# Performance work log

Measured on AMD Instinct MI355X. Metric: run time of the kernel, lower is better.

## Reference

```python
import jax, jax.numpy as jnp
import numpy as np

D_MODEL = 1024
EXPERT_SIZE = 512
N_EXPERTS = 8
GROUP_SIZE = 32
BATCH = 32
SEQ = 2048
TEMPERATURE = 1.0


def setup_inputs() -> dict:
    key = jax.random.key(0)
    k_x, k_l1, k_l2, k_c = jax.random.split(key, 4)
    x = jax.random.normal(k_x, (BATCH, SEQ, D_MODEL), dtype=jnp.float32)
    # truncated-normal-style init approximated with normal scaled by 1/sqrt(fan_in)
    lin1 = jax.random.normal(k_l1, (N_EXPERTS, D_MODEL, EXPERT_SIZE), dtype=jnp.float32) * (D_MODEL ** -0.5)
    lin2 = jax.random.normal(k_l2, (N_EXPERTS, EXPERT_SIZE, D_MODEL), dtype=jnp.float32) * (EXPERT_SIZE ** -0.5)
    controller = jax.random.normal(k_c, (D_MODEL, N_EXPERTS), dtype=jnp.float32) * (D_MODEL ** -0.5)
    return {"x": x, "lin1": lin1, "lin2": lin2, "controller": controller}


def reference(x, lin1, lin2, controller):
    B, S, D = x.shape
    # group_tokens: sparsity_dim=0 -> transpose to (S, B, D), split batch into groups
    xg = jnp.transpose(x, (1, 0, 2)).reshape(S, B // GROUP_SIZE, GROUP_SIZE, D)  # (s, g, k, d)
    # controller logits, softmax over the group (token) axis k (dim=-2)
    logits = jnp.einsum("sgkd,de->sgke", xg, controller) / TEMPERATURE
    merge_w = jax.nn.softmax(logits, axis=-2)  # (s, g, k, e)
    emit_w = merge_w  # default: emit softmax over tokens, same temp -> reuse
    # merge: weighted sum of tokens per expert
    merged = jnp.einsum("sgke,sgkd->sged", merge_w, xg)  # (s, g, e, d)
    # per-expert MLP
    h = jax.nn.relu(jnp.einsum("sged,edf->sgef", merged, lin1))  # (s, g, e, f)
    expert_out = jnp.einsum("sgef,efd->sged", h, lin2)  # (s, g, e, d)
    # emit back to tokens
    out = jnp.einsum("sgke,sged->sgkd", emit_w, expert_out)  # (s, g, k, d)
    # redistribute: (S, B, D) -> (B, S, D)
    return jnp.transpose(out.reshape(S, B, D), (1, 0, 2))
```

## Files before the change

### kernel.cpp

```cpp
#include <hip/hip_runtime.h>
#include <hip/hip_bf16.h>

#define SS 2048
#define BB 32
#define DD 1024
#define FF 512
#define EE 8

typedef __attribute__((ext_vector_type(8))) short short8;
typedef __attribute__((ext_vector_type(8))) unsigned short ushort8v;
typedef __attribute__((ext_vector_type(4))) unsigned short ushort4v;
typedef __attribute__((ext_vector_type(4))) float f32x4;

__device__ inline unsigned short f2bf(float f) {
  union { float f; unsigned u; } v; v.f = f;
  return (unsigned short)((v.u + 0x7FFFu + ((v.u >> 16) & 1u)) >> 16);
}
__device__ inline float bf2f(unsigned short h) {
  union { unsigned u; float f; } v; v.u = ((unsigned)h) << 16;
  return v.f;
}

__global__ __launch_bounds__(256) void transpose_bf16(
    const float* __restrict__ in, unsigned short* __restrict__ out, int K, int N) {
  __shared__ float tile[32][33];
  int e = blockIdx.z;
  const float* inp = in + (size_t)e * K * N;
  unsigned short* outp = out + (size_t)e * K * N;
  int k0 = blockIdx.x * 32, n0 = blockIdx.y * 32;
  int tx = threadIdx.x;
  int ty = threadIdx.y;
#pragma unroll
  for (int i = 0; i < 4; i++) {
    int k = ty + i * 8;
    tile[k][tx] = inp[(size_t)(k0 + k) * N + n0 + tx];
  }
  __syncthreads();
#pragma unroll
  for (int i = 0; i < 4; i++) {
    int n = ty + i * 8;
    outp[(size_t)(n0 + n) * K + k0 + tx] = f2bf(tile[tx][n]);
  }
}

__global__ __launch_bounds__(512) void ctrl_merge(
    const float* __restrict__ x,
    const float* __restrict__ ctrl,
    unsigned short* __restrict__ merged,
    float* __restrict__ mw) {
  int s = blockIdx.x;
  int t = threadIdx.x;
  int lane = t & 63, w = t >> 6;

  __shared__ float cs[EE][DD];
  __shared__ unsigned short xs[BB][DD];
  __shared__ float wl[BB][EE];

  for (int i = t; i < DD * EE; i += 512) {
    int e2 = i >> 10, d = i & 1023;
    cs[e2][d] = ctrl[(size_t)d * EE + e2];
  }
  __syncthreads();

  float acc[4][8] = {};
#pragma unroll
  for (int i = 0; i < 4; i++) {
    int dbase = lane * 4 + i * 256;
    float4 c4[8];
#pragma unroll
    for (int e2 = 0; e2 < 8; e2++) c4[e2] = *(const float4*)&cs[e2][dbase];
#pragma unroll
    for (int kk = 0; kk < 4; kk++) {
      int k = (w << 2) + kk;
      float4 xv = *(const float4*)&x[((size_t)k * SS + s) * DD + dbase];
      ushort4v pv;
      pv[0] = f2bf(xv.x); pv[1] = f2bf(xv.y); pv[2] = f2bf(xv.z); pv[3] = f2bf(xv.w);
      *(ushort4v*)&xs[k][dbase] = pv;
#pragma unroll
      for (int e2 = 0; e2 < 8; e2++)
        acc[kk][e2] += xv.x * c4[e2].x + xv.y * c4[e2].y + xv.z * c4[e2].z + xv.w * c4[e2].w;
    }
  }
#pragma unroll
  for (int off = 1; off < 64; off <<= 1)
#pragma unroll
    for (int kk = 0; kk < 4; kk++)
#pragma unroll
      for (int e2 = 0; e2 < 8; e2++)
        acc[kk][e2] += __shfl_xor(acc[kk][e2], off, 64);
  if (lane == 0) {
#pragma unroll
    for (int kk = 0; kk < 4; kk++)
#pragma unroll
      for (int e2 = 0; e2 < 8; e2++)
        wl[(w << 2) + kk][e2] = acc[kk][e2];
  }
  __syncthreads();

  if (t < 32) {
    float lgv[8], mx[8], p[8], sm[8];
#pragma unroll
    for (int e2 = 0; e2 < 8; e2++) { lgv[e2] = wl[t][e2]; mx[e2] = lgv[e2]; }
#pragma unroll
    for (int off = 1; off < 32; off <<= 1)
#pragma unroll
      for (int e2 = 0; e2 < 8; e2++)
        mx[e2] = fmaxf(mx[e2], __shfl_xor(mx[e2], off, 64));
#pragma unroll
    for (int e2 = 0; e2 < 8; e2++) { p[e2] = __expf(lgv[e2] - mx[e2]); sm[e2] = p[e2]; }
#pragma unroll
    for (int off = 1; off < 32; off <<= 1)
#pragma unroll
      for (int e2 = 0; e2 < 8; e2++)
        sm[e2] += __shfl_xor(sm[e2], off, 64);
    float wv[8];
#pragma unroll
    for (int e2 = 0; e2 < 8; e2++) { wv[e2] = p[e2] / sm[e2]; wl[t][e2] = wv[e2]; }
    float4 mv0 = {wv[0], wv[1], wv[2], wv[3]};
    float4 mv1 = {wv[4], wv[5], wv[6], wv[7]};
    float* mwp = &mw[((size_t)s * BB + t) * EE];
    *(float4*)mwp = mv0;
    *(float4*)(mwp + 4) = mv1;
  }
  __syncthreads();

  int d0 = t << 1;
  float a0[8] = {}, a1[8] = {};
#pragma unroll 4
  for (int k = 0; k < 32; k++) {
    unsigned xv = *(const unsigned*)&xs[k][d0];
    float x0 = bf2f((unsigned short)xv);
    float x1 = bf2f((unsigned short)(xv >> 16));
    float4 wA = *(const float4*)&wl[k][0];
    float4 wB = *(const float4*)&wl[k][4];
    a0[0] += wA.x * x0; a1[0] += wA.x * x1;
    a0[1] += wA.y * x0; a1[1] += wA.y * x1;
    a0[2] += wA.z * x0; a1[2] += wA.z * x1;
    a0[3] += wA.w * x0; a1[3] += wA.w * x1;
    a0[4] += wB.x * x0; a1[4] += wB.x * x1;
    a0[5] += wB.y * x0; a1[5] += wB.y * x1;
    a0[6] += wB.z * x0; a1[6] += wB.z * x1;
    a0[7] += wB.w * x0; a1[7] += wB.w * x1;
  }
#pragma unroll
  for (int e2 = 0; e2 < 8; e2++) {
    unsigned pm = (unsigned)f2bf(a0[e2]) | ((unsigned)f2bf(a1[e2]) << 16);
    *(unsigned*)&merged[((size_t)s * EE + e2) * DD + d0] = pm;
  }
}

template <int RELU>
__global__ __launch_bounds__(256) void gemm_bt(
    const unsigned short* __restrict__ A, const unsigned short* __restrict__ Bt,
    unsigned short* __restrict__ C, int K, int N) {
  int e = blockIdx.z;
  int m0 = blockIdx.x * 128;
  int n0 = blockIdx.y * 128;
  const int lda = EE * K;
  const unsigned short* Ae = A + (size_t)e * K;
  const unsigned short* Be = Bt + (size_t)e * N * K;

  __shared__ __align__(16) unsigned short As[128][40];
  __shared__ __align__(16) unsigned short Bs[128][40];

  int t = threadIdx.x;
  int lane = t & 63, w = t >> 6;
  int wm = w >> 1, wn = w & 1;
  int lr = lane & 15;
  int kh = lane >> 4;

  f32x4 acc[4][4] = {};

  for (int kt = 0; kt < K; kt += 32) {
#pragma unroll
    for (int i = 0; i < 2; i++) {
      int o = t + i * 256;
      int r = o >> 2, c8 = (o & 3) * 8;
      ushort8v va = *(const ushort8v*)&Ae[(size_t)(m0 + r) * lda + kt + c8];
      *(ushort8v*)&As[r][c8] = va;
      ushort8v vb = *(const ushort8v*)&Be[(size_t)(n0 + r) * K + kt + c8];
      *(ushort8v*)&Bs[r][c8] = vb;
    }
    __syncthreads();

    short8 af[4], bfr[4];
#pragma unroll
    for (int mi = 0; mi < 4; mi++)
      af[mi] = *(const short8*)&As[wm * 64 + mi * 16 + lr][kh * 8];
#pragma unroll
    for (int ni = 0; ni < 4; ni++)
      bfr[ni] = *(const short8*)&Bs[wn * 64 + ni * 16 + lr][kh * 8];
#pragma unroll
    for (int mi = 0; mi < 4; mi++)
#pragma unroll
      for (int ni = 0; ni < 4; ni++)
        acc[mi][ni] = __builtin_amdgcn_mfma_f32_16x16x32_bf16(af[mi], bfr[ni], acc[mi][ni], 0, 0, 0);
    __syncthreads();
  }

  int rb = (lane >> 4) * 4;
  int cb = lane & 15;
#pragma unroll
  for (int mi = 0; mi < 4; mi++)
#pragma unroll
    for (int ni = 0; ni < 4; ni++)
#pragma unroll
      for (int r = 0; r < 4; r++) {
        float v = acc[mi][ni][r];
        if (RELU) v = fmaxf(v, 0.f);
        int m = m0 + wm * 64 + mi * 16 + rb + r;
        int n = n0 + wn * 64 + ni * 16 + cb;
        C[(size_t)m * (EE * N) + (size_t)e * N + n] = f2bf(v);
      }
}

__global__ __launch_bounds__(256) void emit_out(
    const unsigned short* __restrict__ eo,
    const float* __restrict__ mw,
    float* __restrict__ out) {
  int s = blockIdx.x;
  int t = threadIdx.x;
  __shared__ float wsm[BB][EE];
  wsm[t >> 3][t & 7] = mw[(size_t)s * BB * EE + t];
  __syncthreads();
  int d0 = t * 4;
  float ev[EE][4];
#pragma unroll
  for (int e2 = 0; e2 < 8; e2++) {
    ushort4v v = *(const ushort4v*)&eo[((size_t)s * EE + e2) * DD + d0];
    ev[e2][0] = bf2f(v[0]); ev[e2][1] = bf2f(v[1]);
    ev[e2][2] = bf2f(v[2]); ev[e2][3] = bf2f(v[3]);
  }
  for (int b = 0; b < BB; b++) {
    float o0 = 0.f, o1 = 0.f, o2 = 0.f, o3 = 0.f;
#pragma unroll
    for (int e2 = 0; e2 < 8; e2++) {
      float we = wsm[b][e2];
      o0 += we * ev[e2][0]; o1 += we * ev[e2][1];
      o2 += we * ev[e2][2]; o3 += we * ev[e2][3];
    }
    float4 ov = {o0, o1, o2, o3};
    *(float4*)&out[((size_t)b * SS + s) * DD + d0] = ov;
  }
}

extern "C" void kernel_launch(void* const* d_in, const int* in_sizes, int n_in,
                              void* d_out, int out_size, void* d_ws, size_t ws_size,
                              hipStream_t stream) {
  const float* x = (const float*)d_in[0];
  const float* lin1 = (const float*)d_in[1];
  const float* lin2 = (const float*)d_in[2];
  const float* ctrl = (const float*)d_in[3];
  float* out = (float*)d_out;

  char* ws = (char*)d_ws;
  size_t off = 0;
  unsigned short* lin1t = (unsigned short*)(ws + off); off += (size_t)EE * DD * FF * 2;
  unsigned short* lin2t = (unsigned short*)(ws + off); off += (size_t)EE * FF * DD * 2;
  unsigned short* merged = (unsigned short*)(ws + off); off += (size_t)SS * EE * DD * 2;
  unsigned short* hbuf = (unsigned short*)(ws + off); off += (size_t)SS * EE * FF * 2;
  unsigned short* eo = (unsigned short*)(ws + off); off += (size_t)SS * EE * DD * 2;
  float* mw = (float*)(ws + off); off += (size_t)SS * BB * EE * 4;

  dim3 tb(32, 8);
  transpose_bf16<<<dim3(DD / 32, FF / 32, EE), tb, 0, stream>>>(lin1, lin1t, DD, FF);
  transpose_bf16<<<dim3(FF / 32, DD / 32, EE), tb, 0, stream>>>(lin2, lin2t, FF, DD);

  ctrl_merge<<<SS, 512, 0, stream>>>(x, ctrl, merged, mw);

  gemm_bt<1><<<dim3(SS / 128, FF / 128, EE), 256, 0, stream>>>(merged, lin1t, hbuf, DD, FF);
  gemm_bt<0><<<dim3(SS / 128, DD / 128, EE), 256, 0, stream>>>(hbuf, lin2t, eo, FF, DD);

  emit_out<<<SS, 256, 0, stream>>>(eo, mw, out);
}
```

Baseline: 328.0 us.

## Split controller/merge kernel and use direct global-to-LDS loads in GEMM

The fused ctrl_merge kernel is split into ctrl_logits and softmax_merge. The controller weights are pre-transposed once so the LDS fill is coalesced, and the merge re-reads x in fp32 from global instead of caching bf16 x in LDS. This cuts LDS use and raises occupancy, at the cost of reading x (256MB) twice. Separately, the bf16 GEMM now loads tiles with global_load_lds into an XOR-swizzled, unpadded LDS layout to avoid register staging and bank conflicts.

```diff
diff --git a/kernel.cpp b/kernel.cpp
--- a/kernel.cpp
+++ b/kernel.cpp
@@ -19,6 +19,13 @@
 __device__ inline float bf2f(unsigned short h) {
   union { unsigned u; float f; } v; v.u = ((unsigned)h) << 16;
   return v.f;
+}
+
+__global__ __launch_bounds__(256) void ctrl_transpose(
+    const float* __restrict__ ctrl, float* __restrict__ ctrlT) {
+  int i = blockIdx.x * 256 + threadIdx.x;
+  int e = i >> 10, d = i & 1023;
+  ctrlT[i] = ctrl[(size_t)d * EE + e];
 }
 
 __global__ __launch_bounds__(256) void transpose_bf16(
@@ -43,79 +50,82 @@
   }
 }
 
-__global__ __launch_bounds__(512) void ctrl_merge(
+__global__ __launch_bounds__(512) void ctrl_logits(
     const float* __restrict__ x,
-    const float* __restrict__ ctrl,
+    const float* __restrict__ ctrlT,
+    float* __restrict__ lg) {
+  int s = blockIdx.x;
+  int t = threadIdx.x, lane = t & 63, w = t >> 6;
+  __shared__ __align__(16) float cs[EE * DD];
+  for (int i = t; i < EE * DD / 4; i += 512)
+    *(float4*)&cs[i * 4] = *(const float4*)&ctrlT[i * 4];
+  __syncthreads();
+
+  float acc[4][8] = {};
+#pragma unroll
+  for (int i = 0; i < 4; i++) {
+    int dbase = lane * 4 + i * 256;
+    float4 c4[8];
+#pragma unroll
+    for (int e = 0; e < 8; e++) c4[e] = *(const float4*)&cs[e * DD + dbase];
+#pragma unroll
+    for (int j = 0; j < 4; j++) {
+      int k = w * 4 + j;
+      float4 xv = *(const float4*)&x[((size_t)k * SS + s) * DD + dbase];
+#pragma unroll
+      for (int e = 0; e < 8; e++)
+        acc[j][e] += xv.x * c4[e].x + xv.y * c4[e].y + xv.z * c4[e].z + xv.w * c4[e].w;
+    }
+  }
+#pragma unroll
+  for (int off = 1; off < 64; off <<= 1)
+#pragma unroll
+    for (int j = 0; j < 4; j++)
+#pragma unroll
+      for (int e = 0; e < 8; e++)
+        acc[j][e] += __shfl_xor(acc[j][e], off, 64);
+  if (lane == 0) {
+#pragma unroll
+    for (int j = 0; j < 4; j++) {
+      int k = w * 4 + j;
+      float4 lo = {acc[j][0], acc[j][1], acc[j][2], acc[j][3]};
+      float4 hi = {acc[j][4], acc[j][5], acc[j][6], acc[j][7]};
+      float* p = &lg[((size_t)s * BB + k) * EE];
+      *(float4*)p = lo;
+      *(float4*)(p + 4) = hi;
+    }
+  }
+}
+
+__global__ __launch_bounds__(256) void softmax_merge(
+    const float* __restrict__ x,
+    const float* __restrict__ lg,
     unsigned short* __restrict__ merged,
     float* __restrict__ mw) {
   int s = blockIdx.x;
   int t = threadIdx.x;
-  int lane = t & 63, w = t >> 6;
-
-  __shared__ float cs[EE][DD];
-  __shared__ unsigned short xs[BB][DD];
-  __shared__ float wl[BB][EE];
-
-  for (int i = t; i < DD * EE; i += 512) {
-    int e2 = i >> 10, d = i & 1023;
-    cs[e2][d] = ctrl[(size_t)d * EE + e2];
-  }
-  __syncthreads();
-
-  float acc[4][8] = {};
-#pragma unroll
-  for (int i = 0; i < 4; i++) {
-    int dbase = lane * 4 + i * 256;
-    float4 c4[8];
-#pragma unroll
-    for (int e2 = 0; e2 < 8; e2++) c4[e2] = *(const float4*)&cs[e2][dbase];
-#pragma unroll
-    for (int kk = 0; kk < 4; kk++) {
-      int k = (w << 2) + kk;
-      float4 xv = *(const float4*)&x[((size_t)k * SS + s) * DD + dbase];
-      ushort4v pv;
-      pv[0] = f2bf(xv.x); pv[1] = f2bf(xv.y); pv[2] = f2bf(xv.z); pv[3] = f2bf(xv.w);
-      *(ushort4v*)&xs[k][dbase] = pv;
-#pragma unroll
-      for (int e2 = 0; e2 < 8; e2++)
-        acc[kk][e2] += xv.x * c4[e2].x + xv.y * c4[e2].y + xv.z * c4[e2].z + xv.w * c4[e2].w;
-    }
-  }
-#pragma unroll
-  for (int off = 1; off < 64; off <<= 1)
-#pragma unroll
-    for (int kk = 0; kk < 4; kk++)
-#pragma unroll
-      for (int e2 = 0; e2 < 8; e2++)
-        acc[kk][e2] += __shfl_xor(acc[kk][e2], off, 64);
-  if (lane == 0) {
-#pragma unroll
-    for (int kk = 0; kk < 4; kk++)
-#pragma unroll
-      for (int e2 = 0; e2 < 8; e2++)
-        wl[(w << 2) + kk][e2] = acc[kk][e2];
-  }
-  __syncthreads();
-
+  __shared__ __align__(16) float wl[BB][EE];
+  wl[t >> 3][t & 7] = lg[(size_t)s * BB * EE + t];
+  __syncthreads();
   if (t < 32) {
     float lgv[8], mx[8], p[8], sm[8];
 #pragma unroll
-    for (int e2 = 0; e2 < 8; e2++) { lgv[e2] = wl[t][e2]; mx[e2] = lgv[e2]; }
+    for (int e = 0; e < 8; e++) { lgv[e] = wl[t][e]; mx[e] = lgv[e]; }
 #pragma unroll
     for (int off = 1; off < 32; off <<= 1)
 #pragma unroll
-      for (int e2 = 0; e2 < 8; e2++)
-        mx[e2] = fmaxf(mx[e2], __shfl_xor(mx[e2], off, 64));
-#pragma unroll
-    for (int e2 = 0; e2 < 8; e2++) { p[e2] = __expf(lgv[e2] - mx[e2]); sm[e2] = p[e2]; }
+      for (int e = 0; e < 8; e++)
+        mx[e] = fmaxf(mx[e], __shfl_xor(mx[e], off, 64));
+#pragma unroll
+    for (int e = 0; e < 8; e++) { p[e] = __expf(lgv[e] - mx[e]); sm[e] = p[e]; }
 #pragma unroll
     for (int off = 1; off < 32; off <<= 1)
 #pragma unroll
-      for (int e2 = 0; e2 < 8; e2++)
-        sm[e2] += __shfl_xor(sm[e2], off, 64);
+      for (int e = 0; e < 8; e++)
+        sm[e] += __shfl_xor(sm[e], off, 64);
     float wv[8];
 #pragma unroll
-    for (int e2 = 0; e2 < 8; e2++) { wv[e2] = p[e2] / sm[e2]; wl[t][e2] = wv[e2]; }
+    for (int e = 0; e < 8; e++) { wv[e] = p[e] / sm[e]; wl[t][e] = wv[e]; }
     float4 mv0 = {wv[0], wv[1], wv[2], wv[3]};
     float4 mv1 = {wv[4], wv[5], wv[6], wv[7]};
     float* mwp = &mw[((size_t)s * BB + t) * EE];
@@ -124,28 +134,28 @@
   }
   __syncthreads();
 
-  int d0 = t << 1;
-  float a0[8] = {}, a1[8] = {};
+  int d0 = t * 4;
+  float a[8][4] = {};
 #pragma unroll 4
   for (int k = 0; k < 32; k++) {
-    unsigned xv = *(const unsigned*)&xs[k][d0];
-    float x0 = bf2f((unsigned short)xv);
-    float x1 = bf2f((unsigned short)(xv >> 16));
+    float4 xv = *(const float4*)&x[((size_t)k * SS + s) * DD + d0];
     float4 wA = *(const float4*)&wl[k][0];
     float4 wB = *(const float4*)&wl[k][4];
-    a0[0] += wA.x * x0; a1[0] += wA.x * x1;
-    a0[1] += wA.y * x0; a1[1] += wA.y * x1;
-    a0[2] += wA.z * x0; a1[2] += wA.z * x1;
-    a0[3] += wA.w * x0; a1[3] += wA.w * x1;
-    a0[4] += wB.x * x0; a1[4] += wB.x * x1;
-    a0[5] += wB.y * x0; a1[5] += wB.y * x1;
-    a0[6] += wB.z * x0; a1[6] += wB.z * x1;
-    a0[7] += wB.w * x0; a1[7] += wB.w * x1;
-  }
-#pragma unroll
-  for (int e2 = 0; e2 < 8; e2++) {
-    unsigned pm = (unsigned)f2bf(a0[e2]) | ((unsigned)f2bf(a1[e2]) << 16);
-    *(unsigned*)&merged[((size_t)s * EE + e2) * DD + d0] = pm;
+    a[0][0] += wA.x * xv.x; a[0][1] += wA.x * xv.y; a[0][2] += wA.x * xv.z; a[0][3] += wA.x * xv.w;
+    a[1][0] += wA.y * xv.x; a[1][1] += wA.y * xv.y; a[1][2] += wA.y * xv.z; a[1][3] += wA.y * xv.w;
+    a[2][0] += wA.z * xv.x; a[2][1] += wA.z * xv.y; a[2][2] += wA.z * xv.z; a[2][3] += wA.z * xv.w;
+    a[3][0] += wA.w * xv.x; a[3][1] += wA.w * xv.y; a[3][2] += wA.w * xv.z; a[3][3] += wA.w * xv.w;
+    a[4][0] += wB.x * xv.x; a[4][1] += wB.x * xv.y; a[4][2] += wB.x * xv.z; a[4][3] += wB.x * xv.w;
+    a[5][0] += wB.y * xv.x; a[5][1] += wB.y * xv.y; a[5][2] += wB.y * xv.z; a[5][3] += wB.y * xv.w;
+    a[6][0] += wB.z * xv.x; a[6][1] += wB.z * xv.y; a[6][2] += wB.z * xv.z; a[6][3] += wB.z * xv.w;
+    a[7][0] += wB.w * xv.x; a[7][1] += wB.w * xv.y; a[7][2] += wB.w * xv.z; a[7][3] += wB.w * xv.w;
+  }
+#pragma unroll
+  for (int e = 0; e < 8; e++) {
+    ushort4v pv;
+    pv[0] = f2bf(a[e][0]); pv[1] = f2bf(a[e][1]);
+    pv[2] = f2bf(a[e][2]); pv[3] = f2bf(a[e][3]);
+    *(ushort4v*)&merged[((size_t)s * EE + e) * DD + d0] = pv;
   }
 }
 
@@ -160,36 +170,40 @@
   const unsigned short* Ae = A + (size_t)e * K;
   const unsigned short* Be = Bt + (size_t)e * N * K;
 
-  __shared__ __align__(16) unsigned short As[128][40];
-  __shared__ __align__(16) unsigned short Bs[128][40];
+  __shared__ __align__(16) unsigned short As[128 * 32];
+  __shared__ __align__(16) unsigned short Bs[128 * 32];
 
   int t = threadIdx.x;
   int lane = t & 63, w = t >> 6;
   int wm = w >> 1, wn = w & 1;
   int lr = lane & 15;
   int kh = lane >> 4;
+  int khs = kh ^ ((lr >> 1) & 3);
 
   f32x4 acc[4][4] = {};
 
   for (int kt = 0; kt < K; kt += 32) {
 #pragma unroll
     for (int i = 0; i < 2; i++) {
-      int o = t + i * 256;
-      int r = o >> 2, c8 = (o & 3) * 8;
-      ushort8v va = *(const ushort8v*)&Ae[(size_t)(m0 + r) * lda + kt + c8];
-      *(ushort8v*)&As[r][c8] = va;
-      ushort8v vb = *(const ushort8v*)&Be[(size_t)(n0 + r) * K + kt + c8];
-      *(ushort8v*)&Bs[r][c8] = vb;
+      int c = t + i * 256;
+      int r = c >> 2;
+      int subg = (c & 3) ^ ((r >> 1) & 3);
+      __builtin_amdgcn_global_load_lds(
+          (const __attribute__((address_space(1))) void*)(Ae + (size_t)(m0 + r) * lda + kt + subg * 8),
+          (__attribute__((address_space(3))) void*)(&As[c * 8]), 16, 0, 0);
+      __builtin_amdgcn_global_load_lds(
+          (const __attribute__((address_space(1))) void*)(Be + (size_t)(n0 + r) * K + kt + subg * 8),
+          (__attribute__((address_space(3))) void*)(&Bs[c * 8]), 16, 0, 0);
     }
     __syncthreads();
 
     short8 af[4], bfr[4];
 #pragma unroll
     for (int mi = 0; mi < 4; mi++)
-      af[mi] = *(const short8*)&As[wm * 64 + mi * 16 + lr][kh * 8];
+      af[mi] = *(const short8*)&As[(wm * 64 + mi * 16 + lr) * 32 + khs * 8];
 #pragma unroll
     for (int ni = 0; ni < 4; ni++)
-      bfr[ni] = *(const short8*)&Bs[wn * 64 + ni * 16 + lr][kh * 8];
+      bfr[ni] = *(const short8*)&Bs[(wn * 64 + ni * 16 + lr) * 32 + khs * 8];
 #pragma unroll
     for (int mi = 0; mi < 4; mi++)
 #pragma unroll
@@ -261,12 +275,17 @@
   unsigned short* hbuf = (unsigned short*)(ws + off); off += (size_t)SS * EE * FF * 2;
   unsigned short* eo = (unsigned short*)(ws + off); off += (size_t)SS * EE * DD * 2;
   float* mw = (float*)(ws + off); off += (size_t)SS * BB * EE * 4;
+  float* lg = (float*)(ws + off); off += (size_t)SS * BB * EE * 4;
+  float* ctrlT = (float*)(ws + off); off += (size_t)EE * DD * 4;
+
+  ctrl_transpose<<<32, 256, 0, stream>>>(ctrl, ctrlT);
 
   dim3 tb(32, 8);
   transpose_bf16<<<dim3(DD / 32, FF / 32, EE), tb, 0, stream>>>(lin1, lin1t, DD, FF);
   transpose_bf16<<<dim3(FF / 32, DD / 32, EE), tb, 0, stream>>>(lin2, lin2t, FF, DD);
 
-  ctrl_merge<<<SS, 512, 0, stream>>>(x, ctrl, merged, mw);
+  ctrl_logits<<<SS, 512, 0, stream>>>(x, ctrlT, lg);
+  softmax_merge<<<SS, 256, 0, stream>>>(x, lg, merged, mw);
 
   gemm_bt<1><<<dim3(SS / 128, FF / 128, EE), 256, 0, stream>>>(merged, lin1t, hbuf, DD, FF);
   gemm_bt<0><<<dim3(SS / 128, DD / 128, EE), 256, 0, stream>>>(hbuf, lin2t, eo, FF, DD);
```

Result: slower. 337.5 us (+2.9%).
